# Performance work log

Hardware: AMD Instinct MI355X
Metric: run time of the kernel (lower is better)

Reference implementation:

```python
import jax, jax.numpy as jnp
import numpy as np


def setup_inputs() -> dict:
    key = jax.random.key(0)
    k1, k2 = jax.random.split(key)
    b, feat = 8192, 256
    x = jax.random.normal(k1, (b, feat), dtype=jnp.float32)
    y = jax.random.randint(k2, (b,), 0, 100, dtype=jnp.int64)
    T = jnp.zeros((1,), dtype=jnp.float32)
    return {"x": x, "y": y, "T": T}


def reference(x, y, T):
    # SNNLoss.forward with inv=False, d=None, and no -1 labels in y
    b = x.shape[0]
    x = x / jnp.std(x, ddof=1)  # torch .std() is unbiased (ddof=1)

    # Pairwise Euclidean distance via Gram matrix (avoids [b,b,feat] blowup)
    sq = jnp.sum(x * x, axis=1)  # [b]
    d2 = jnp.maximum(sq[:, None] + sq[None, :] - 2.0 * (x @ x.T), 0.0)  # [b,b]
    eye = jnp.eye(b, dtype=bool)
    # diagonal is exactly 0 and masked out later; keep sqrt grad-safe there
    dist = jnp.where(eye, 0.0, jnp.sqrt(jnp.where(eye, 1.0, d2)))

    e_dist = -dist * jnp.power(jnp.float32(10.0), T[0])  # [b,b]
    neg_inf = jnp.float32(-jnp.inf)

    # denominator: all pairs except self
    den_dist = jnp.where(eye, neg_inf, e_dist)
    den = jax.scipy.special.logsumexp(den_dist, axis=1)  # [b]

    # numerator: same-label pairs except self
    m_num = (y[:, None] == y[None, :]) & ~eye  # [b,b]
    has = jnp.any(m_num, axis=1)  # rows with at least one positive
    num_dist = jnp.where(m_num, e_dist, neg_inf)
    # rows with no positives would give logsumexp = -inf; torch code zeroes
    # both num and den there. Substitute finite values, then zero the term.
    num = jax.scipy.special.logsumexp(jnp.where(has[:, None], num_dist, 0.0), axis=1)
    terms = jnp.where(has, num - den, 0.0)
    return -jnp.mean(terms)
```

## Files before the change

kernel.cpp:

```cpp
#include <hip/hip_runtime.h>

#define B_ROWS 8192
#define FEAT   256
#define NCH    16
#define CH_COLS 512
#define NJT    8

typedef float f32x4 __attribute__((ext_vector_type(4)));
typedef _Float16 f16x8 __attribute__((ext_vector_type(8)));

typedef const __attribute__((address_space(1))) unsigned int* gas_ptr;
typedef __attribute__((address_space(3))) unsigned int* las_ptr;

__device__ __forceinline__ void gload_lds16(const void* g, void* l) {
  __builtin_amdgcn_global_load_lds((gas_ptr)g, (las_ptr)l, 16, 0, 0);
}

__global__ __launch_bounds__(256) void prep_kernel(
    const float* __restrict__ x, unsigned short* __restrict__ xh,
    float* __restrict__ sq, float* __restrict__ part_s,
    float* __restrict__ part_q)
{
  int tid = threadIdx.x;
  int l = tid & 63, wid = tid >> 6;
  int row = blockIdx.x * 4 + wid;
  const float4* xv = (const float4*)(x + (size_t)row * FEAT);
  float4 v = xv[l];
  ushort4 u;
  u.x = __builtin_bit_cast(unsigned short, (_Float16)v.x);
  u.y = __builtin_bit_cast(unsigned short, (_Float16)v.y);
  u.z = __builtin_bit_cast(unsigned short, (_Float16)v.z);
  u.w = __builtin_bit_cast(unsigned short, (_Float16)v.w);
  ((ushort4*)(xh + (size_t)row * FEAT))[l] = u;
  float ssq  = v.x*v.x + v.y*v.y + v.z*v.z + v.w*v.w;
  float ssum = v.x + v.y + v.z + v.w;
  #pragma unroll
  for (int m = 32; m; m >>= 1) {
    ssq  += __shfl_xor(ssq, m);
    ssum += __shfl_xor(ssum, m);
  }
  if (l == 0) sq[row] = ssq;
  __shared__ float red[8];
  if (l == 0) { red[wid*2] = ssum; red[wid*2+1] = ssq; }
  __syncthreads();
  if (tid == 0) {
    part_s[blockIdx.x] = red[0]+red[2]+red[4]+red[6];
    part_q[blockIdx.x] = red[1]+red[3]+red[5]+red[7];
  }
}

template<bool DIAG>
__device__ __forceinline__ void epilogue(
    const f32x4 (&acc)[2][4], const float* __restrict__ sq,
    const int* __restrict__ y, int j0, int l15,
    int i0q, const float (&sqi)[8], const int (&yiv)[8],
    float (&sden)[8], float (&snum)[8], float nscale2)
{
  int jb = j0 + l15;
  float sqj[4]; int yj[4];
  #pragma unroll
  for (int cb = 0; cb < 4; ++cb) {
    int j = jb + cb*16;
    sqj[cb] = sq[j];
    yj[cb]  = y[j];
  }
  #pragma unroll
  for (int rb = 0; rb < 2; ++rb) {
    #pragma unroll
    for (int r = 0; r < 4; ++r) {
      float si = sqi[rb*4+r];
      int   ig = i0q + rb*16 + r;
      int   yi = yiv[rb*4+r];
      float dacc = 0.f, nacc = 0.f;
      #pragma unroll
      for (int cb = 0; cb < 4; ++cb) {
        float S  = acc[rb][cb][r];
        float d2 = fmaf(S, -2.0f, si + sqj[cb]);
        d2 = fmaxf(d2, 0.0f);
        float e  = __builtin_amdgcn_exp2f(__builtin_amdgcn_sqrtf(d2) * nscale2);
        bool offd = !DIAG || (ig != jb + cb*16);
        dacc += offd ? e : 0.0f;
        nacc += (yi == yj[cb] && offd) ? e : 0.0f;
      }
      sden[rb*4+r] += dacc;
      snum[rb*4+r] += nacc;
    }
  }
}

__global__ __launch_bounds__(256, 2) void snn_main(
    const unsigned short* __restrict__ xh, const float* __restrict__ sq,
    const int* __restrict__ y, const float* __restrict__ T,
    const float* __restrict__ part_s, const float* __restrict__ part_q,
    float* __restrict__ pden, float* __restrict__ pnum)
{
  __shared__ __align__(16) char lB[32768];
  int tid = threadIdx.x;
  int l = tid & 63, wid = tid >> 6;
  int quad = l >> 4, l15 = l & 15;
  int l5 = l >> 5, s31 = l & 31;
  int ch = blockIdx.x, it = blockIdx.y;
  int i0 = it * 128, chbase = ch * CH_COLS;
  const char* xbc = (const char*)xh;

  f16x8 areg[2][8];
  #pragma unroll
  for (int rb = 0; rb < 2; ++rb)
    #pragma unroll
    for (int kk = 0; kk < 8; ++kk)
      areg[rb][kk] = *(const f16x8*)(xbc +
          (size_t)(i0 + wid*32 + rb*16 + l15)*512 + kk*64 + quad*16);

  float s_acc = 0.f, q_acc = 0.f;
  #pragma unroll
  for (int t = 0; t < 32; ++t) {
    s_acc += part_s[l + 64*t];
    q_acc += part_q[l + 64*t];
  }
  #pragma unroll
  for (int m = 1; m <= 32; m <<= 1) {
    s_acc += __shfl_xor(s_acc, m);
    q_acc += __shfl_xor(q_acc, m);
  }
  const double n = (double)B_ROWS * FEAT;
  double var = ((double)q_acc - (double)s_acc*(double)s_acc/n) / (n - 1.0);
  float stdv = (float)sqrt(var);
  float p10  = __builtin_amdgcn_exp2f(T[0] * 3.3219280948873623f);
  float nscale2 = -(p10 * 1.4426950408889634f / stdv);

  float sqi[8]; int yiv[8];
  int i0q = i0 + wid*32 + quad*4;
  #pragma unroll
  for (int rb = 0; rb < 2; ++rb)
    #pragma unroll
    for (int r = 0; r < 4; ++r) {
      int idx = i0q + rb*16 + r;
      sqi[rb*4+r] = sq[idx];
      yiv[rb*4+r] = y[idx];
    }

  float sden[8], snum[8];
  #pragma unroll
  for (int v = 0; v < 8; ++v) { sden[v] = 0.f; snum[v] = 0.f; }
  f32x4 acc[2][4];
  const f32x4 zero4 = {0.f, 0.f, 0.f, 0.f};

  for (int jt = 0; jt < NJT; ++jt) {
    int j0 = chbase + jt * 64;

    __syncthreads();
    {
      const char* gB = xbc + (size_t)j0 * 512;
      #pragma unroll
      for (int s = 0; s < 8; ++s) {
        int c  = wid*8 + s;
        int rw = 2*c + l5;
        int gg = s31 ^ (rw & 7);
        gload_lds16(gB + rw*512 + gg*16, lB + c*1024);
      }
    }

    if (jt > 0) {
      int pj0 = j0 - 64;
      if (pj0 == i0 || pj0 == i0 + 64)
        epilogue<true >(acc, sq, y, pj0, l15, i0q, sqi, yiv, sden, snum, nscale2);
      else
        epilogue<false>(acc, sq, y, pj0, l15, i0q, sqi, yiv, sden, snum, nscale2);
    }
    #pragma unroll
    for (int rb = 0; rb < 2; ++rb)
      #pragma unroll
      for (int cb = 0; cb < 4; ++cb)
        acc[rb][cb] = zero4;

    __syncthreads();

    #pragma unroll
    for (int kk = 0; kk < 8; ++kk) {
      f16x8 bv[4];
      #pragma unroll
      for (int cb = 0; cb < 4; ++cb) {
        int nr = cb*16 + l15;
        bv[cb] = *(const f16x8*)(lB + nr*512 + ((((kk<<2)|quad) ^ (l15 & 7)) << 4));
      }
      #pragma unroll
      for (int rb = 0; rb < 2; ++rb)
        #pragma unroll
        for (int cb = 0; cb < 4; ++cb)
          acc[rb][cb] = __builtin_amdgcn_mfma_f32_16x16x32_f16(areg[rb][kk], bv[cb], acc[rb][cb], 0, 0, 0);
    }
  }
  {
    int pj0 = chbase + (NJT-1) * 64;
    if (pj0 == i0 || pj0 == i0 + 64)
      epilogue<true >(acc, sq, y, pj0, l15, i0q, sqi, yiv, sden, snum, nscale2);
    else
      epilogue<false>(acc, sq, y, pj0, l15, i0q, sqi, yiv, sden, snum, nscale2);
  }

  #pragma unroll
  for (int v = 0; v < 8; ++v) {
    #pragma unroll
    for (int m = 1; m <= 8; m <<= 1) {
      sden[v] += __shfl_xor(sden[v], m);
      snum[v] += __shfl_xor(snum[v], m);
    }
  }
  if (l15 == 0) {
    int base = (it*NCH + ch) * 128;
    #pragma unroll
    for (int rb = 0; rb < 2; ++rb)
      #pragma unroll
      for (int r = 0; r < 4; ++r) {
        int rin = wid*32 + rb*16 + quad*4 + r;
        pden[base + rin] = sden[rb*4+r];
        pnum[base + rin] = snum[rb*4+r];
      }
  }
}

__global__ __launch_bounds__(1024) void final_kernel(
    const float* __restrict__ pden, const float* __restrict__ pnum,
    float* __restrict__ out)
{
  int tid = threadIdx.x;
  float tot = 0.f;
  #pragma unroll
  for (int rr = 0; rr < 8; ++rr) {
    int row = tid + 1024*rr;
    int itt = row >> 7, rin = row & 127;
    float den = 0.f, num = 0.f;
    #pragma unroll
    for (int p = 0; p < NCH; ++p) {
      den += pden[(itt*NCH + p)*128 + rin];
      num += pnum[(itt*NCH + p)*128 + rin];
    }
    if (num > 0.f)
      tot += 0.6931471805599453f *
             (__builtin_amdgcn_logf(num) - __builtin_amdgcn_logf(den));
  }
  #pragma unroll
  for (int m = 32; m; m >>= 1) tot += __shfl_xor(tot, m);
  __shared__ float red[16];
  if ((tid & 63) == 0) red[tid >> 6] = tot;
  __syncthreads();
  if (tid == 0) {
    float s = 0.f;
    #pragma unroll
    for (int w = 0; w < 16; ++w) s += red[w];
    out[0] = -s / 8192.0f;
  }
}

extern "C" void kernel_launch(void* const* d_in, const int* in_sizes, int n_in,
                              void* d_out, int out_size, void* d_ws, size_t ws_size,
                              hipStream_t stream)
{
  (void)in_sizes; (void)n_in; (void)out_size; (void)ws_size;
  const float* x  = (const float*)d_in[0];
  const int* y    = (const int*)d_in[1];
  const float* T  = (const float*)d_in[2];
  char* ws = (char*)d_ws;
  float* part_s = (float*)(ws + 1024);
  float* part_q = (float*)(ws + 1024 + 8192);
  float* sq     = (float*)(ws + 32768);
  unsigned short* xh = (unsigned short*)(ws + 65536);
  float* pden   = (float*)(ws + 65536 + 4194304);
  float* pnum   = pden + 64*NCH*128;

  hipLaunchKernelGGL(prep_kernel, dim3(B_ROWS/4), dim3(256), 0, stream,
                     x, xh, sq, part_s, part_q);
  hipLaunchKernelGGL(snn_main, dim3(NCH, B_ROWS/128), dim3(256), 0, stream,
                     xh, sq, y, T, part_s, part_q, pden, pnum);
  hipLaunchKernelGGL(final_kernel, dim3(1), dim3(1024), 0, stream,
                     pden, pnum, (float*)d_out);
}
```

Before: 128.0 us.

## Exploit distance-matrix symmetry: compute upper-triangle tiles, accumulate column sums atomically

The pairwise distance matrix is symmetric, so the main kernel now visits only the j-tiles on or above each 128-row block's diagonal. Column-wise partial denominators and numerators from off-diagonal tiles are reduced across the wave and added into per-row global accumulators with atomics. Those accumulators are zeroed in the prep kernel, and the final kernel adds them to the row partials. This roughly halves MFMA and exp work, at the cost of atomic traffic and uneven per-block work across row tiles, which the reversed row-tile ordering tries to offset.

Result: faster. 121.6 us (-5.0%).

```diff
diff --git a/kernel.cpp b/kernel.cpp
--- a/kernel.cpp
+++ b/kernel.cpp
@@ -2,9 +2,8 @@
 
 #define B_ROWS 8192
 #define FEAT   256
-#define NCH    16
-#define CH_COLS 512
-#define NJT    8
+#define NCCH   8
+#define NJTILE 128
 
 typedef float f32x4 __attribute__((ext_vector_type(4)));
 typedef _Float16 f16x8 __attribute__((ext_vector_type(8)));
@@ -19,7 +18,8 @@
 __global__ __launch_bounds__(256) void prep_kernel(
     const float* __restrict__ x, unsigned short* __restrict__ xh,
     float* __restrict__ sq, float* __restrict__ part_s,
-    float* __restrict__ part_q)
+    float* __restrict__ part_q, float* __restrict__ col_den,
+    float* __restrict__ col_num)
 {
   int tid = threadIdx.x;
   int l = tid & 63, wid = tid >> 6;
@@ -32,6 +32,11 @@
   u.z = __builtin_bit_cast(unsigned short, (_Float16)v.z);
   u.w = __builtin_bit_cast(unsigned short, (_Float16)v.w);
   ((ushort4*)(xh + (size_t)row * FEAT))[l] = u;
+  if (tid < 4) {
+    int r4 = blockIdx.x * 4 + tid;
+    col_den[r4] = 0.f;
+    col_num[r4] = 0.f;
+  }
   float ssq  = v.x*v.x + v.y*v.y + v.z*v.z + v.w*v.w;
   float ssum = v.x + v.y + v.z + v.w;
   #pragma unroll
@@ -49,12 +54,13 @@
   }
 }
 
-template<bool DIAG>
+template<bool DIAG, bool COL>
 __device__ __forceinline__ void epilogue(
     const f32x4 (&acc)[2][4], const float* __restrict__ sq,
-    const int* __restrict__ y, int j0, int l15,
+    const int* __restrict__ y, int j0, int l15, int l,
     int i0q, const float (&sqi)[8], const int (&yiv)[8],
-    float (&sden)[8], float (&snum)[8], float nscale2)
+    float (&sden)[8], float (&snum)[8], float nscale2,
+    float* __restrict__ col_den, float* __restrict__ col_num)
 {
   int jb = j0 + l15;
   float sqj[4]; int yj[4];
@@ -63,6 +69,11 @@
     int j = jb + cb*16;
     sqj[cb] = sq[j];
     yj[cb]  = y[j];
+  }
+  float cd[4], cn[4];
+  if (COL) {
+    #pragma unroll
+    for (int cb = 0; cb < 4; ++cb) { cd[cb] = 0.f; cn[cb] = 0.f; }
   }
   #pragma unroll
   for (int rb = 0; rb < 2; ++rb) {
@@ -78,12 +89,33 @@
         float d2 = fmaf(S, -2.0f, si + sqj[cb]);
         d2 = fmaxf(d2, 0.0f);
         float e  = __builtin_amdgcn_exp2f(__builtin_amdgcn_sqrtf(d2) * nscale2);
+        bool same = (yi == yj[cb]);
         bool offd = !DIAG || (ig != jb + cb*16);
         dacc += offd ? e : 0.0f;
-        nacc += (yi == yj[cb] && offd) ? e : 0.0f;
+        nacc += (same && offd) ? e : 0.0f;
+        if (COL) {
+          cd[cb] += e;
+          cn[cb] += same ? e : 0.0f;
+        }
       }
       sden[rb*4+r] += dacc;
       snum[rb*4+r] += nacc;
+    }
+  }
+  if (COL) {
+    #pragma unroll
+    for (int cb = 0; cb < 4; ++cb) {
+      cd[cb] += __shfl_xor(cd[cb], 16);
+      cd[cb] += __shfl_xor(cd[cb], 32);
+      cn[cb] += __shfl_xor(cn[cb], 16);
+      cn[cb] += __shfl_xor(cn[cb], 32);
+    }
+    if (l < 16) {
+      #pragma unroll
+      for (int cb = 0; cb < 4; ++cb) {
+        atomicAdd(&col_den[j0 + cb*16 + l], cd[cb]);
+        atomicAdd(&col_num[j0 + cb*16 + l], cn[cb]);
+      }
     }
   }
 }
@@ -92,15 +124,17 @@
     const unsigned short* __restrict__ xh, const float* __restrict__ sq,
     const int* __restrict__ y, const float* __restrict__ T,
     const float* __restrict__ part_s, const float* __restrict__ part_q,
-    float* __restrict__ pden, float* __restrict__ pnum)
+    float* __restrict__ pden, float* __restrict__ pnum,
+    float* __restrict__ col_den, float* __restrict__ col_num)
 {
   __shared__ __align__(16) char lB[32768];
   int tid = threadIdx.x;
   int l = tid & 63, wid = tid >> 6;
   int quad = l >> 4, l15 = l & 15;
   int l5 = l >> 5, s31 = l & 31;
-  int ch = blockIdx.x, it = blockIdx.y;
-  int i0 = it * 128, chbase = ch * CH_COLS;
+  int c = blockIdx.x, yb = blockIdx.y;
+  int it = (yb < 32) ? yb : 95 - yb;
+  int i0 = it * 128;
   const char* xbc = (const char*)xh;
 
   f16x8 areg[2][8];
@@ -145,27 +179,32 @@
   f32x4 acc[2][4];
   const f32x4 zero4 = {0.f, 0.f, 0.f, 0.f};
 
-  for (int jt = 0; jt < NJT; ++jt) {
-    int j0 = chbase + jt * 64;
+  int f = 2*it + ((c - 2*it) & 7);
+  int pjt = -1;
+
+  for (int jt = f; jt < NJTILE; jt += 8) {
+    int j0 = jt * 64;
 
     __syncthreads();
     {
       const char* gB = xbc + (size_t)j0 * 512;
       #pragma unroll
       for (int s = 0; s < 8; ++s) {
-        int c  = wid*8 + s;
-        int rw = 2*c + l5;
+        int cc = wid*8 + s;
+        int rw = 2*cc + l5;
         int gg = s31 ^ (rw & 7);
-        gload_lds16(gB + rw*512 + gg*16, lB + c*1024);
-      }
-    }
-
-    if (jt > 0) {
-      int pj0 = j0 - 64;
-      if (pj0 == i0 || pj0 == i0 + 64)
-        epilogue<true >(acc, sq, y, pj0, l15, i0q, sqi, yiv, sden, snum, nscale2);
+        gload_lds16(gB + rw*512 + gg*16, lB + cc*1024);
+      }
+    }
+
+    if (pjt >= 0) {
+      int pj0 = pjt * 64;
+      if ((pjt >> 1) == it)
+        epilogue<true , false>(acc, sq, y, pj0, l15, l, i0q, sqi, yiv,
+                               sden, snum, nscale2, col_den, col_num);
       else
-        epilogue<false>(acc, sq, y, pj0, l15, i0q, sqi, yiv, sden, snum, nscale2);
+        epilogue<false, true >(acc, sq, y, pj0, l15, l, i0q, sqi, yiv,
+                               sden, snum, nscale2, col_den, col_num);
     }
     #pragma unroll
     for (int rb = 0; rb < 2; ++rb)
@@ -189,13 +228,16 @@
         for (int cb = 0; cb < 4; ++cb)
           acc[rb][cb] = __builtin_amdgcn_mfma_f32_16x16x32_f16(areg[rb][kk], bv[cb], acc[rb][cb], 0, 0, 0);
     }
-  }
-  {
-    int pj0 = chbase + (NJT-1) * 64;
-    if (pj0 == i0 || pj0 == i0 + 64)
-      epilogue<true >(acc, sq, y, pj0, l15, i0q, sqi, yiv, sden, snum, nscale2);
+    pjt = jt;
+  }
+  if (pjt >= 0) {
+    int pj0 = pjt * 64;
+    if ((pjt >> 1) == it)
+      epilogue<true , false>(acc, sq, y, pj0, l15, l, i0q, sqi, yiv,
+                             sden, snum, nscale2, col_den, col_num);
     else
-      epilogue<false>(acc, sq, y, pj0, l15, i0q, sqi, yiv, sden, snum, nscale2);
+      epilogue<false, true >(acc, sq, y, pj0, l15, l, i0q, sqi, yiv,
+                             sden, snum, nscale2, col_den, col_num);
   }
 
   #pragma unroll
@@ -207,7 +249,7 @@
     }
   }
   if (l15 == 0) {
-    int base = (it*NCH + ch) * 128;
+    int base = (it*NCCH + c) * 128;
     #pragma unroll
     for (int rb = 0; rb < 2; ++rb)
       #pragma unroll
@@ -221,6 +263,7 @@
 
 __global__ __launch_bounds__(1024) void final_kernel(
     const float* __restrict__ pden, const float* __restrict__ pnum,
+    const float* __restrict__ col_den, const float* __restrict__ col_num,
     float* __restrict__ out)
 {
   int tid = threadIdx.x;
@@ -229,11 +272,11 @@
   for (int rr = 0; rr < 8; ++rr) {
     int row = tid + 1024*rr;
     int itt = row >> 7, rin = row & 127;
-    float den = 0.f, num = 0.f;
-    #pragma unroll
-    for (int p = 0; p < NCH; ++p) {
-      den += pden[(itt*NCH + p)*128 + rin];
-      num += pnum[(itt*NCH + p)*128 + rin];
+    float den = col_den[row], num = col_num[row];
+    #pragma unroll
+    for (int p = 0; p < NCCH; ++p) {
+      den += pden[(itt*NCCH + p)*128 + rin];
+      num += pnum[(itt*NCCH + p)*128 + rin];
     }
     if (num > 0.f)
       tot += 0.6931471805599453f *
@@ -266,12 +309,14 @@
   float* sq     = (float*)(ws + 32768);
   unsigned short* xh = (unsigned short*)(ws + 65536);
   float* pden   = (float*)(ws + 65536 + 4194304);
-  float* pnum   = pden + 64*NCH*128;
+  float* pnum   = pden + 64*NCCH*128;
+  float* col_den = pnum + 64*NCCH*128;
+  float* col_num = col_den + B_ROWS;
 
   hipLaunchKernelGGL(prep_kernel, dim3(B_ROWS/4), dim3(256), 0, stream,
-                     x, xh, sq, part_s, part_q);
-  hipLaunchKernelGGL(snn_main, dim3(NCH, B_ROWS/128), dim3(256), 0, stream,
-                     xh, sq, y, T, part_s, part_q, pden, pnum);
+                     x, xh, sq, part_s, part_q, col_den, col_num);
+  hipLaunchKernelGGL(snn_main, dim3(NCCH, B_ROWS/128), dim3(256), 0, stream,
+                     xh, sq, y, T, part_s, part_q, pden, pnum, col_den, col_num);
   hipLaunchKernelGGL(final_kernel, dim3(1), dim3(1024), 0, stream,
-                     pden, pnum, (float*)d_out);
-}
+                     pden, pnum, col_den, col_num, (float*)d_out);
+}
```
